# Kernel optimization log

Measured on AMD Instinct MI355X. Metric: run time of the kernel, lower is better.

Reference implementation:

```python
import jax, jax.numpy as jnp
import numpy as np

V, D, H, F, L, M, T, B, MAXT = 32000, 1024, 16, 4096, 3, 1, 1024, 2, 2048
HD = D // H

def _ln(x, g, b, eps=1e-5):
    m = x.mean(-1, keepdims=True)
    v = ((x - m) ** 2).mean(-1, keepdims=True)
    return (x - m) * jax.lax.rsqrt(v + eps) * g + b

def _mha(x, Wq, bq, Wk, bk, Wv, bv, Wo, bo, mask):
    Bx, Tx, Dx = x.shape
    q = (x @ Wq.T + bq).reshape(Bx, Tx, H, HD)
    k = (x @ Wk.T + bk).reshape(Bx, Tx, H, HD)
    v = (x @ Wv.T + bv).reshape(Bx, Tx, H, HD)
    s = jnp.einsum('bqhd,bkhd->bhqk', q, k) / np.float32(np.sqrt(HD))
    s = jnp.where(mask[None, None], s, jnp.float32(-1e9))
    a = jax.nn.softmax(s, axis=-1)
    o = jnp.einsum('bhqk,bkhd->bqhd', a, v).reshape(Bx, Tx, Dx)
    return o @ Wo.T + bo

def setup_inputs() -> dict:
    key = jax.random.key(0)
    ks = iter(jax.random.split(key, 64))
    rn = lambda shape: jax.random.normal(next(ks), shape, jnp.float32) * 0.02
    inp = {
        'x': jax.random.randint(next(ks), (B, T), 0, V),
        'mask': jnp.tril(jnp.ones((T, T), bool)),  # causal mask
        'tok_W': rn((V, D)),  # embedding table = Linear(V,D).weight.T
        'pos_embed': rn((MAXT, D)),
        'Wq': rn((L, D, D)), 'bq': jnp.zeros((L, D)),
        'Wk': rn((L, D, D)), 'bk': jnp.zeros((L, D)),
        'Wv': rn((L, D, D)), 'bv': jnp.zeros((L, D)),
        'Wo': rn((L, D, D)), 'bo': jnp.zeros((L, D)),
        'ln1_g': jnp.ones((L, D)), 'ln1_b': jnp.zeros((L, D)),
        'W1': rn((L, F, D)), 'b1': jnp.zeros((L, F)),
        'W2': rn((L, D, F)), 'b2': jnp.zeros((L, D)),
        'ln2_g': jnp.ones((L, D)), 'ln2_b': jnp.zeros((L, D)),
        'mWq': rn((M, D, D)), 'mbq': jnp.zeros((M, D)),
        'mWk': rn((M, D, D)), 'mbk': jnp.zeros((M, D)),
        'mWv': rn((M, D, D)), 'mbv': jnp.zeros((M, D)),
        'mWo': rn((M, D, D)), 'mbo': jnp.zeros((M, D)),
        'mln_g': jnp.ones((M, D)), 'mln_b': jnp.zeros((M, D)),
        'tWq': rn((D, D)), 'tbq': jnp.zeros((D,)),
        'tWk': rn((D, D)), 'tbk': jnp.zeros((D,)),
        'tWv': rn((D, D)), 'tbv': jnp.zeros((D,)),
        'tWo': rn((D, D)), 'tbo': jnp.zeros((D,)),
        'tln_g': jnp.ones((D,)), 'tln_b': jnp.zeros((D,)),
        'norm_g': jnp.ones((D,)), 'norm_b': jnp.zeros((D,)),
        'out_W': rn((V, D)), 'out_b': jnp.zeros((V,)),
    }
    return inp

def reference(x, mask, tok_W, pos_embed, Wq, bq, Wk, bk, Wv, bv, Wo, bo,
              ln1_g, ln1_b, W1, b1, W2, b2, ln2_g, ln2_b,
              mWq, mbq, mWk, mbk, mWv, mbv, mWo, mbo, mln_g, mln_b,
              tWq, tbq, tWk, tbk, tWv, tbv, tWo, tbo, tln_g, tln_b,
              norm_g, norm_b, out_W, out_b):
    Bx, Tx = x.shape
    # one_hot(x, V).float() @ W_tok^T  ==  gather row x from the (V, D) table
    h = jnp.take(tok_W, x, axis=0) + pos_embed[:Tx][None]
    mi = 0
    for i in range(L):  # static small layer count
        a = _mha(h, Wq[i], bq[i], Wk[i], bk[i], Wv[i], bv[i], Wo[i], bo[i], mask)
        h = _ln(h + a, ln1_g[i], ln1_b[i])
        f = jax.nn.gelu(h @ W1[i].T + b1[i]) @ W2[i].T + b2[i]
        h = _ln(h + f, ln2_g[i], ln2_b[i])
        if i % 3 == 2 and mi < M:  # memory layer every 3rd block
            a = _mha(h, mWq[mi], mbq[mi], mWk[mi], mbk[mi], mWv[mi], mbv[mi], mWo[mi], mbo[mi], mask)
            h = _ln(h + a, mln_g[mi], mln_b[mi])
            mi += 1
    a = _mha(h, tWq, tbq, tWk, tbk, tWv, tbv, tWo, tbo, mask)  # thought attention
    h = _ln(h + a, tln_g, tln_b)
    h = _ln(h, norm_g, norm_b)
    return h @ out_W.T + out_b  # [B, T, V] logits
```

## Files before the change

kernel.cpp:

```cpp
#include <hip/hip_runtime.h>
#include <cstdint>

#define DEV static __device__ __forceinline__

typedef unsigned short u16;
typedef __attribute__((ext_vector_type(8))) short short8;
typedef __attribute__((ext_vector_type(4))) float f32x4;

namespace cfg {
constexpr int V = 32000, D = 1024, H = 16, F = 4096, L = 3, T = 1024, B = 2;
constexpr int N = B * T;
constexpr int HD = D / H;
}

DEV float bf2f(u16 b) { union { unsigned u; float f; } x; x.u = (unsigned)b << 16; return x.f; }
DEV u16 f2bf(float f) {
  union { float f; unsigned u; } x; x.f = f;
  unsigned u = x.u;
  return (u16)((u + 0x7fffu + ((u >> 16) & 1u)) >> 16);
}

DEV void gload16(void* lds, const void* g) {
  __builtin_amdgcn_global_load_lds((__attribute__((address_space(1))) void*)g,
                                   (__attribute__((address_space(3))) void*)lds, 16, 0, 0);
}

DEV float waveSum(float v) {
#pragma unroll
  for (int o = 32; o; o >>= 1) v += __shfl_xor(v, o);
  return v;
}

struct CastJob { const float* src; u16* dst; int nBlk; };
struct CastArgs { CastJob j[24]; int n; };

__global__ void cast_kernel(CastArgs a) {
  int blk = blockIdx.x;
  int i = 0;
  while (i + 1 < a.n && blk >= a.j[i].nBlk) { blk -= a.j[i].nBlk; ++i; }
  const size_t base = (size_t)blk * 2048 + threadIdx.x * 8;
  const float4* s4 = (const float4*)(a.j[i].src + base);
  const float4 v0 = s4[0], v1 = s4[1];
  short8 o;
  o[0] = (short)f2bf(v0.x); o[1] = (short)f2bf(v0.y);
  o[2] = (short)f2bf(v0.z); o[3] = (short)f2bf(v0.w);
  o[4] = (short)f2bf(v1.x); o[5] = (short)f2bf(v1.y);
  o[6] = (short)f2bf(v1.z); o[7] = (short)f2bf(v1.w);
  *(short8*)(a.j[i].dst + base) = o;
}

struct CopyJob { const float* src; float* dst; };
struct CopyArgs { CopyJob j[16]; int n; };
__global__ void bconcat_kernel(CopyArgs a) {
  const CopyJob jb = a.j[blockIdx.x];
  ((float4*)jb.dst)[threadIdx.x] = ((const float4*)jb.src)[threadIdx.x];
}

__global__ void embed_kernel(const int* __restrict__ x, const float* __restrict__ tokW,
                             const float* __restrict__ pos, float* __restrict__ hF,
                             u16* __restrict__ hB) {
  const int bt = blockIdx.x;
  const int t = bt & (cfg::T - 1);
  const int tid = threadIdx.x;
  const int idx = x[bt];
  float4 v = ((const float4*)(tokW + (size_t)idx * cfg::D))[tid];
  const float4 p = ((const float4*)(pos + (size_t)t * cfg::D))[tid];
  v.x += p.x; v.y += p.y; v.z += p.z; v.w += p.w;
  ((float4*)(hF + (size_t)bt * cfg::D))[tid] = v;
  union { u16 u[4]; uint2 q; } pk;
  pk.u[0] = f2bf(v.x); pk.u[1] = f2bf(v.y); pk.u[2] = f2bf(v.z); pk.u[3] = f2bf(v.w);
  *(uint2*)(hB + (size_t)bt * cfg::D + tid * 4) = pk.q;
}

template <int NADD>
__global__ void ln_kernel(const float* __restrict__ base,
                          const float* __restrict__ a0, const float* __restrict__ a1,
                          const float* __restrict__ a2, const float* __restrict__ a3,
                          const float* __restrict__ biasv,
                          const float* __restrict__ g, const float* __restrict__ bt,
                          float* __restrict__ outF, u16* __restrict__ outB) {
  const int row = blockIdx.x, tid = threadIdx.x;
  const int lane = tid & 63, wid = tid >> 6;
  const size_t roff = (size_t)row * cfg::D;
  float4 x = ((const float4*)(base + roff))[tid];
  if (NADD >= 1) {
    const float4 a = ((const float4*)(a0 + roff))[tid];
    x.x += a.x; x.y += a.y; x.z += a.z; x.w += a.w;
  }
  if (NADD >= 2) {
    const float4 a = ((const float4*)(a1 + roff))[tid];
    x.x += a.x; x.y += a.y; x.z += a.z; x.w += a.w;
  }
  if (NADD >= 3) {
    const float4 a = ((const float4*)(a2 + roff))[tid];
    x.x += a.x; x.y += a.y; x.z += a.z; x.w += a.w;
  }
  if (NADD >= 4) {
    const float4 a = ((const float4*)(a3 + roff))[tid];
    x.x += a.x; x.y += a.y; x.z += a.z; x.w += a.w;
  }
  if (biasv) {
    const float4 a = ((const float4*)biasv)[tid];
    x.x += a.x; x.y += a.y; x.z += a.z; x.w += a.w;
  }
  float s = x.x + x.y + x.z + x.w;
  float s2 = x.x * x.x + x.y * x.y + x.z * x.z + x.w * x.w;
  __shared__ float sb[8];
  s = waveSum(s); s2 = waveSum(s2);
  if (lane == 0) { sb[wid] = s; sb[4 + wid] = s2; }
  __syncthreads();
  s = sb[0] + sb[1] + sb[2] + sb[3];
  s2 = sb[4] + sb[5] + sb[6] + sb[7];
  const float mean = s * (1.f / cfg::D);
  const float rs = rsqrtf(s2 * (1.f / cfg::D) - mean * mean + 1e-5f);
  const float4 gv = ((const float4*)g)[tid];
  const float4 bv = ((const float4*)bt)[tid];
  float4 y;
  y.x = (x.x - mean) * rs * gv.x + bv.x;
  y.y = (x.y - mean) * rs * gv.y + bv.y;
  y.z = (x.z - mean) * rs * gv.z + bv.z;
  y.w = (x.w - mean) * rs * gv.w + bv.w;
  ((float4*)(outF + roff))[tid] = y;
  union { u16 u[4]; uint2 q; } pk;
  pk.u[0] = f2bf(y.x); pk.u[1] = f2bf(y.y); pk.u[2] = f2bf(y.z); pk.u[3] = f2bf(y.w);
  *(uint2*)(outB + roff + tid * 4) = pk.q;
}

__global__ void vtrans_kernel(const u16* __restrict__ v, u16* __restrict__ vtO, int vstride) {
  __shared__ u16 s[64][68];
  const int bh = blockIdx.y, b = bh >> 4, h = bh & 15;
  const int t0 = blockIdx.x * 64;
  const int tid = threadIdx.x;
  const int r2 = tid >> 3, cg = tid & 7;
#pragma unroll
  for (int p = 0; p < 2; ++p) {
    const int r = p * 32 + r2;
    const short8 val = *(const short8*)(v + (size_t)(b * cfg::T + t0 + r) * vstride + h * 64 + cg * 8);
#pragma unroll
    for (int j = 0; j < 8; ++j) s[r][cg * 8 + j] = (u16)val[j];
  }
  __syncthreads();
#pragma unroll
  for (int p = 0; p < 2; ++p) {
    const int d = p * 32 + r2;
    short8 o;
#pragma unroll
    for (int j = 0; j < 8; ++j) o[j] = (short)s[cg * 8 + j][d];
    *(short8*)(vtO + ((size_t)bh * 64 + d) * (size_t)cfg::T + t0 + cg * 8) = o;
  }
}

template <int NCH>
DEV void stageTile(u16* lds, const u16* src, int strideElems, int tid) {
#pragma unroll
  for (int c = 0; c < NCH / 256; ++c) {
    const int ci = c * 256 + tid;
    const int r = ci >> 3;
    const int c8 = ci & 7;
    const int sc8 = c8 ^ (r & 7);
    gload16(lds + (size_t)ci * 8, src + (size_t)r * strideElems + sc8 * 8);
  }
}
DEV short8 ldsFrag(const u16* tile, int row, int kElem) {
  const int byteoff = row * 128 + ((kElem * 2) ^ ((row & 7) << 4));
  return *(const short8*)((const char*)tile + byteoff);
}

__launch_bounds__(256, 3)
__global__ void fattn_kernel(const u16* __restrict__ qkv, const u16* __restrict__ vt,
                             u16* __restrict__ o) {
  constexpr int D3 = 3 * cfg::D;
  __shared__ u16 Qs[64 * 64];
  __shared__ u16 Ks[64 * 64];
  __shared__ u16 Vs[64 * 64];
  __shared__ u16 Ps[64][72];
  const int tid = threadIdx.x, lane = tid & 63, w = tid >> 6;
  const int qt = gridDim.x - 1 - blockIdx.x;
  const int bh = blockIdx.y;
  const int b = bh >> 4, h = bh & 15;
  const int q0 = qt * 64;
  const int l15 = lane & 15, lq = lane >> 4;

  stageTile<512>(Qs, qkv + (size_t)(b * cfg::T + q0) * D3 + h * 64, D3, tid);
  __syncthreads();
  short8 qf[2];
#pragma unroll
  for (int kk = 0; kk < 2; ++kk)
    qf[kk] = ldsFrag(Qs, w * 16 + l15, kk * 32 + lq * 8);

  f32x4 oa[4];
  float m[4], l[4];
#pragma unroll
  for (int r = 0; r < 4; ++r) { m[r] = -1e30f; l[r] = 0.f; }
#pragma unroll
  for (int nt = 0; nt < 4; ++nt) { oa[nt][0] = 0; oa[nt][1] = 0; oa[nt][2] = 0; oa[nt][3] = 0; }

  const int nkt = qt + 1;
  const u16* kbase = qkv + (size_t)(b * cfg::T) * D3 + cfg::D + h * 64;
  const u16* vbase = vt + (size_t)bh * 64 * cfg::T;

  for (int kt = 0; kt < nkt; ++kt) {
    const int k0 = kt * 64;
    __syncthreads();
    stageTile<512>(Ks, kbase + (size_t)k0 * D3, D3, tid);
    stageTile<512>(Vs, vbase + k0, cfg::T, tid);
    __syncthreads();

    f32x4 sa[4];
#pragma unroll
    for (int nt = 0; nt < 4; ++nt) { sa[nt][0] = 0; sa[nt][1] = 0; sa[nt][2] = 0; sa[nt][3] = 0; }
#pragma unroll
    for (int kk = 0; kk < 2; ++kk) {
      short8 kf[4];
#pragma unroll
      for (int nt = 0; nt < 4; ++nt) kf[nt] = ldsFrag(Ks, nt * 16 + l15, kk * 32 + lq * 8);
#pragma unroll
      for (int nt = 0; nt < 4; ++nt)
        sa[nt] = __builtin_amdgcn_mfma_f32_16x16x32_bf16(qf[kk], kf[nt], sa[nt], 0, 0, 0);
    }

    const bool needMask = (kt >= qt);
#pragma unroll
    for (int r = 0; r < 4; ++r) {
      const int qrow = q0 + w * 16 + lq * 4 + r;
      float s[4];
#pragma unroll
      for (int nt = 0; nt < 4; ++nt) {
        s[nt] = sa[nt][r] * 0.125f;
        if (needMask && (k0 + nt * 16 + l15 > qrow)) s[nt] = -3e38f;
      }
      float rm = fmaxf(fmaxf(s[0], s[1]), fmaxf(s[2], s[3]));
#pragma unroll
      for (int off = 1; off < 16; off <<= 1) rm = fmaxf(rm, __shfl_xor(rm, off));
      const float mn = fmaxf(m[r], rm);
      const float sc = __expf(m[r] - mn);
      m[r] = mn;
      float ps = 0.f;
#pragma unroll
      for (int nt = 0; nt < 4; ++nt) {
        const float p = __expf(s[nt] - mn);
        ps += p;
        Ps[w * 16 + lq * 4 + r][nt * 16 + l15] = f2bf(p);
      }
#pragma unroll
      for (int off = 1; off < 16; off <<= 1) ps += __shfl_xor(ps, off);
      l[r] = l[r] * sc + ps;
#pragma unroll
      for (int nt = 0; nt < 4; ++nt) oa[nt][r] *= sc;
    }

#pragma unroll
    for (int kk = 0; kk < 2; ++kk) {
      short8 pa = *(const short8*)&Ps[w * 16 + l15][kk * 32 + lq * 8];
      short8 vf[4];
#pragma unroll
      for (int nt = 0; nt < 4; ++nt) vf[nt] = ldsFrag(Vs, nt * 16 + l15, kk * 32 + lq * 8);
#pragma unroll
      for (int nt = 0; nt < 4; ++nt)
        oa[nt] = __builtin_amdgcn_mfma_f32_16x16x32_bf16(pa, vf[nt], oa[nt], 0, 0, 0);
    }
  }

  u16* obase = o + (size_t)(b * cfg::T + q0 + w * 16) * cfg::D + h * 64;
#pragma unroll
  for (int r = 0; r < 4; ++r) {
    const float inv = 1.f / l[r];
    const int rl = lq * 4 + r;
#pragma unroll
    for (int nt = 0; nt < 4; ++nt)
      obase[(size_t)rl * cfg::D + nt * 16 + l15] = f2bf(oa[nt][r] * inv);
  }
}

template <int BN, int EPI, int OUTF32, int SWZ, int MMAJOR>
__launch_bounds__(256, 4)
__global__ void gemm_kernel(const u16* __restrict__ A, const u16* __restrict__ Bw,
                            const float* __restrict__ bias, void* __restrict__ Cp,
                            int lda, int ldb, int ldc, int K, long long partStride) {
  constexpr int BM = 128, BK = 64;
  constexpr int WN = BN / 2;
  constexpr int MF = 4, NF = WN / 16;
  int bx = blockIdx.x, by = blockIdx.y;
  if (SWZ) {
    const int gx = gridDim.x;
    const int nwg = gx * gridDim.y;
    const int lid = by * gx + bx;
    const int q = nwg >> 3, r = nwg & 7;
    const int xcd = lid & 7, rest = lid >> 3;
    const int nid = (xcd < r ? xcd * (q + 1) : r * (q + 1) + (xcd - r) * q) + rest;
    bx = nid % gx; by = nid / gx;
  }
  const int z = blockIdx.z;
  const u16* Ab = A + (size_t)z * K;
  const u16* Bb = Bw + (size_t)z * K;
  const int tid = threadIdx.x;
  const int lane = tid & 63;
  const int wid = tid >> 6;
  const int wr = wid >> 1, wc = wid & 1;
  const int m0 = (MMAJOR ? bx : by) * BM;
  const int n0 = (MMAJOR ? by : bx) * BN;

  __shared__ u16 As[BM][BK];
  __shared__ u16 Bs[BN][BK];

  const int nkt = K / BK;

  f32x4 acc[MF][NF];
#pragma unroll
  for (int i = 0; i < MF; ++i)
#pragma unroll
    for (int j = 0; j < NF; ++j) {
      acc[i][j][0] = 0.f; acc[i][j][1] = 0.f; acc[i][j][2] = 0.f; acc[i][j][3] = 0.f;
    }

  for (int kt = 0; kt < nkt; ++kt) {
    __syncthreads();
    const int kb = kt * BK;
    stageTile<(BM * BK) / 8>(&As[0][0], Ab + (size_t)m0 * lda + kb, lda, tid);
    stageTile<(BN * BK) / 8>(&Bs[0][0], Bb + (size_t)n0 * ldb + kb, ldb, tid);
    __syncthreads();
#pragma unroll
    for (int kk = 0; kk < BK / 32; ++kk) {
      short8 av[MF], bv[NF];
      const int kElem = kk * 32 + (lane >> 4) * 8;
#pragma unroll
      for (int mt = 0; mt < MF; ++mt)
        av[mt] = ldsFrag(&As[0][0], wr * 64 + mt * 16 + (lane & 15), kElem);
#pragma unroll
      for (int nt = 0; nt < NF; ++nt)
        bv[nt] = ldsFrag(&Bs[0][0], wc * WN + nt * 16 + (lane & 15), kElem);
#pragma unroll
      for (int mt = 0; mt < MF; ++mt)
#pragma unroll
        for (int nt = 0; nt < NF; ++nt)
          acc[mt][nt] = __builtin_amdgcn_mfma_f32_16x16x32_bf16(av[mt], bv[nt], acc[mt][nt], 0, 0, 0);
    }
  }

  const int rhi = (lane >> 4) * 4, cidx = lane & 15;
  const long long cb = (long long)z * partStride;
#pragma unroll
  for (int mt = 0; mt < MF; ++mt) {
#pragma unroll
    for (int nt = 0; nt < NF; ++nt) {
      const int col = n0 + wc * WN + nt * 16 + cidx;
      const float badd = bias ? bias[col] : 0.f;
#pragma unroll
      for (int r = 0; r < 4; ++r) {
        const int row = m0 + wr * 64 + mt * 16 + rhi + r;
        float val = acc[mt][nt][r] + badd;
        if (EPI == 1) {
          const float zz = 1.5957691216057308f * (val + 0.044715f * val * val * val);
          const float th = 1.f - 2.f / (__expf(zz) + 1.f);
          val = 0.5f * val * (1.f + th);
        }
        const size_t off = (size_t)(cb + (long long)row * ldc + col);
        if (OUTF32) ((float*)Cp)[off] = val;
        else ((u16*)Cp)[off] = f2bf(val);
      }
    }
  }
}

extern "C" void kernel_launch(void* const* d_in, const int* in_sizes, int n_in,
                              void* d_out, int out_size, void* d_ws, size_t ws_size,
                              hipStream_t stream) {
  using namespace cfg;
  (void)in_sizes; (void)n_in; (void)out_size;
  const int* x = (const int*)d_in[0];
  const float* tokW = (const float*)d_in[2];
  const float* pos = (const float*)d_in[3];
  const float* Wq = (const float*)d_in[4];  const float* bq = (const float*)d_in[5];
  const float* Wk = (const float*)d_in[6];  const float* bk = (const float*)d_in[7];
  const float* Wv = (const float*)d_in[8];  const float* bv = (const float*)d_in[9];
  const float* Wo = (const float*)d_in[10]; const float* bo = (const float*)d_in[11];
  const float* ln1g = (const float*)d_in[12]; const float* ln1b = (const float*)d_in[13];
  const float* W1 = (const float*)d_in[14]; const float* b1 = (const float*)d_in[15];
  const float* W2 = (const float*)d_in[16]; const float* b2 = (const float*)d_in[17];
  const float* ln2g = (const float*)d_in[18]; const float* ln2b = (const float*)d_in[19];
  const float* mWq = (const float*)d_in[20]; const float* mbq = (const float*)d_in[21];
  const float* mWk = (const float*)d_in[22]; const float* mbk = (const float*)d_in[23];
  const float* mWv = (const float*)d_in[24]; const float* mbv = (const float*)d_in[25];
  const float* mWo = (const float*)d_in[26]; const float* mbo = (const float*)d_in[27];
  const float* mlng = (const float*)d_in[28]; const float* mlnb = (const float*)d_in[29];
  const float* tWq = (const float*)d_in[30]; const float* tbq = (const float*)d_in[31];
  const float* tWk = (const float*)d_in[32]; const float* tbk = (const float*)d_in[33];
  const float* tWv = (const float*)d_in[34]; const float* tbv = (const float*)d_in[35];
  const float* tWo = (const float*)d_in[36]; const float* tbo = (const float*)d_in[37];
  const float* tlng = (const float*)d_in[38]; const float* tlnb = (const float*)d_in[39];
  const float* normg = (const float*)d_in[40]; const float* normb = (const float*)d_in[41];
  const float* outW = (const float*)d_in[42]; const float* outb = (const float*)d_in[43];

  const size_t DD = (size_t)D * D;
  const long long ND = (long long)N * D;
  char* wsb = (char*)d_ws;
  size_t off = 0;
  auto alloc = [&](size_t bytes) {
    void* p = wsb + off;
    off += (bytes + 255) & ~(size_t)255;
    return p;
  };
  u16* qkvW = (u16*)alloc((size_t)L * 3 * DD * 2);
  u16* mqkvW = (u16*)alloc(3 * DD * 2);
  u16* tqkvW = (u16*)alloc(3 * DD * 2);
  u16* WoB = (u16*)alloc((size_t)L * DD * 2);
  u16* W1B = (u16*)alloc((size_t)L * F * D * 2);
  u16* W2B = (u16*)alloc((size_t)L * D * F * 2);
  u16* mWoB = (u16*)alloc(DD * 2);
  u16* tWoB = (u16*)alloc(DD * 2);
  u16* outWB = (u16*)alloc((size_t)V * D * 2);
  float* biasQKV = (float*)alloc((size_t)(L + 2) * 3 * D * 4);
  float* hF = (float*)alloc((size_t)N * D * 4);
  u16* hB = (u16*)alloc((size_t)N * D * 2);
  float* pS = (float*)alloc((size_t)4 * N * D * 4);
  u16* qkvB = (u16*)alloc((size_t)N * 3 * D * 2);
  u16* vtB = (u16*)alloc((size_t)N * D * 2);
  u16* oB = (u16*)alloc((size_t)N * D * 2);
  u16* f1B = (u16*)alloc((size_t)N * F * 2);
  if (off > ws_size) return;

  CastArgs ca;
  int nj = 0; long total = 0;
  auto addJob = [&](const float* s, u16* dptr, size_t n) {
    ca.j[nj].src = s; ca.j[nj].dst = dptr; ca.j[nj].nBlk = (int)(n / 2048);
    total += (long)(n / 2048); ++nj;
  };
  for (int i = 0; i < L; ++i) {
    addJob(Wq + i * DD, qkvW + (size_t)i * 3 * DD, DD);
    addJob(Wk + i * DD, qkvW + (size_t)i * 3 * DD + DD, DD);
    addJob(Wv + i * DD, qkvW + (size_t)i * 3 * DD + 2 * DD, DD);
  }
  addJob(mWq, mqkvW, DD); addJob(mWk, mqkvW + DD, DD); addJob(mWv, mqkvW + 2 * DD, DD);
  addJob(tWq, tqkvW, DD); addJob(tWk, tqkvW + DD, DD); addJob(tWv, tqkvW + 2 * DD, DD);
  addJob(Wo, WoB, (size_t)L * DD);
  addJob(W1, W1B, (size_t)L * F * D);
  addJob(W2, W2B, (size_t)L * D * F);
  addJob(mWo, mWoB, DD); addJob(tWo, tWoB, DD);
  addJob(outW, outWB, (size_t)V * D);
  ca.n = nj;
  cast_kernel<<<dim3((unsigned)total), 256, 0, stream>>>(ca);

  CopyArgs cpa;
  int nc = 0;
  auto addCopy = [&](const float* s, float* dptr) { cpa.j[nc].src = s; cpa.j[nc].dst = dptr; ++nc; };
  for (int i = 0; i < L; ++i) {
    addCopy(bq + (size_t)i * D, biasQKV + (size_t)i * 3 * D);
    addCopy(bk + (size_t)i * D, biasQKV + (size_t)i * 3 * D + D);
    addCopy(bv + (size_t)i * D, biasQKV + (size_t)i * 3 * D + 2 * D);
  }
  addCopy(mbq, biasQKV + (size_t)L * 3 * D); addCopy(mbk, biasQKV + (size_t)L * 3 * D + D);
  addCopy(mbv, biasQKV + (size_t)L * 3 * D + 2 * D);
  addCopy(tbq, biasQKV + (size_t)(L + 1) * 3 * D); addCopy(tbk, biasQKV + (size_t)(L + 1) * 3 * D + D);
  addCopy(tbv, biasQKV + (size_t)(L + 1) * 3 * D + 2 * D);
  cpa.n = nc;
  bconcat_kernel<<<dim3((unsigned)nc), 256, 0, stream>>>(cpa);

  embed_kernel<<<N, 256, 0, stream>>>(x, tokW, pos, hF, hB);

  auto mha = [&](const u16* qkvw, const float* qkvbias, const u16* wo) {
    gemm_kernel<64, 0, 0, 0, 0><<<dim3(3 * D / 64, N / 128, 1), 256, 0, stream>>>(
        hB, qkvw, qkvbias, qkvB, D, D, 3 * D, D, 0);
    vtrans_kernel<<<dim3(T / 64, B * H), 256, 0, stream>>>(qkvB + 2 * D, vtB, 3 * D);
    fattn_kernel<<<dim3(T / 64, B * H), 256, 0, stream>>>(qkvB, vtB, oB);
    gemm_kernel<64, 0, 1, 0, 0><<<dim3(D / 64, N / 128, 4), 256, 0, stream>>>(
        oB, wo, nullptr, pS, D, D, D, 256, ND);
  };
  auto lnMha = [&](const float* obias, const float* g, const float* b_) {
    ln_kernel<4><<<N, 256, 0, stream>>>(hF, pS, pS + ND, pS + 2 * ND, pS + 3 * ND,
                                        obias, g, b_, hF, hB);
  };

  int mi = 0;
  for (int i = 0; i < L; ++i) {
    mha(qkvW + (size_t)i * 3 * DD, biasQKV + (size_t)i * 3 * D, WoB + (size_t)i * DD);
    lnMha(bo + (size_t)i * D, ln1g + (size_t)i * D, ln1b + (size_t)i * D);
    gemm_kernel<64, 1, 0, 0, 0><<<dim3(F / 64, N / 128, 1), 256, 0, stream>>>(
        hB, W1B + (size_t)i * F * D, b1 + (size_t)i * F, f1B, D, D, F, D, 0);
    gemm_kernel<64, 0, 1, 0, 0><<<dim3(D / 64, N / 128, 4), 256, 0, stream>>>(
        f1B, W2B + (size_t)i * D * F, nullptr, pS, F, F, D, 1024, ND);
    ln_kernel<4><<<N, 256, 0, stream>>>(hF, pS, pS + ND, pS + 2 * ND, pS + 3 * ND,
                                        b2 + (size_t)i * D, ln2g + (size_t)i * D,
                                        ln2b + (size_t)i * D, hF, hB);
    if (i % 3 == 2 && mi < 1) {
      mha(mqkvW, biasQKV + (size_t)L * 3 * D, mWoB);
      lnMha(mbo, mlng, mlnb);
      ++mi;
    }
  }
  mha(tqkvW, biasQKV + (size_t)(L + 1) * 3 * D, tWoB);
  lnMha(tbo, tlng, tlnb);
  ln_kernel<0><<<N, 256, 0, stream>>>(hF, nullptr, nullptr, nullptr, nullptr, nullptr,
                                      normg, normb, hF, hB);
  gemm_kernel<128, 0, 1, 1, 1><<<dim3(N / 128, V / 128, 1), 256, 0, stream>>>(
      hB, outWB, outb, (float*)d_out, D, D, V, D, 0);
}
```

Before: 929.2 us.

## Add 256x256-tile 4-stage pipelined GEMM for output logits projection

Adds a new GEMM kernel for the final vocabulary projection. It uses 256x256 tiles, 512 threads, a 4-buffer LDS ring that prefetches 3 stages ahead with explicit vmcnt waits and raw barriers, XCD-aware block remapping, and 16x16x32 bf16 MFMA. The aim is more data reuse per tile and overlap of global loads with MFMA on the largest GEMM. In exchange it needs 128KB of dynamic LDS, which allows only one block per CU. The older kernel is kept as a fallback if the shared-memory attribute cannot be set.

Result: faster. 906.0 us (-2.5%).

```diff
diff --git a/kernel.cpp b/kernel.cpp
--- a/kernel.cpp
+++ b/kernel.cpp
@@ -23,6 +23,23 @@
 DEV void gload16(void* lds, const void* g) {
   __builtin_amdgcn_global_load_lds((__attribute__((address_space(1))) void*)g,
                                    (__attribute__((address_space(3))) void*)lds, 16, 0, 0);
+}
+
+template <int NW>
+DEV void waitVm() {
+  if constexpr (NW == 0) asm volatile("s_waitcnt vmcnt(0)" ::: "memory");
+  else if constexpr (NW == 4) asm volatile("s_waitcnt vmcnt(4)" ::: "memory");
+  else if constexpr (NW == 8) asm volatile("s_waitcnt vmcnt(8)" ::: "memory");
+  __builtin_amdgcn_sched_barrier(0);
+}
+DEV void barrierRaw() {
+  __builtin_amdgcn_sched_barrier(0);
+  __builtin_amdgcn_s_barrier();
+  __builtin_amdgcn_sched_barrier(0);
+}
+DEV void waitLgkm0() {
+  asm volatile("s_waitcnt lgkmcnt(0)" ::: "memory");
+  __builtin_amdgcn_sched_barrier(0);
 }
 
 DEV float waveSum(float v) {
@@ -165,6 +182,10 @@
   const int byteoff = row * 128 + ((kElem * 2) ^ ((row & 7) << 4));
   return *(const short8*)((const char*)tile + byteoff);
 }
+DEV short8 ldsFrag32(const u16* tile, int row, int kElem) {
+  const int byteoff = row * 64 + ((kElem * 2) ^ (((row >> 1) & 3) << 4));
+  return *(const short8*)((const char*)tile + byteoff);
+}
 
 __launch_bounds__(256, 3)
 __global__ void fattn_kernel(const u16* __restrict__ qkv, const u16* __restrict__ vt,
@@ -357,6 +378,107 @@
         const size_t off = (size_t)(cb + (long long)row * ldc + col);
         if (OUTF32) ((float*)Cp)[off] = val;
         else ((u16*)Cp)[off] = f2bf(val);
+      }
+    }
+  }
+}
+
+__launch_bounds__(512, 1)
+__global__ void gemm256c_kernel(const u16* __restrict__ A, const u16* __restrict__ Bw,
+                                const float* __restrict__ bias, float* __restrict__ Cp,
+                                int lda, int ldb, int ldc, int K) {
+  extern __shared__ u16 lds[];
+  int bx = blockIdx.x, by = blockIdx.y;
+  {
+    const int gx = gridDim.x;
+    const int nwg = gx * gridDim.y;
+    const int lid = by * gx + bx;
+    const int q = nwg >> 3, r = nwg & 7;
+    const int xcd = lid & 7, rest = lid >> 3;
+    const int nid = (xcd < r ? xcd * (q + 1) : r * (q + 1) + (xcd - r) * q) + rest;
+    bx = nid % gx; by = nid / gx;
+  }
+  const int tid = threadIdx.x;
+  const int lane = tid & 63;
+  const int wid = tid >> 6;
+  const int wr = wid >> 2, wc = wid & 3;
+  const int m0 = bx * 256;
+  const int n0 = by * 256;
+  const int l15 = lane & 15, lq = lane >> 4;
+
+  const u16* Abase = A + (size_t)m0 * lda;
+  const u16* Bbase = Bw + (size_t)n0 * ldb;
+
+  auto stageHalf = [&](int ldsOff, const u16* srcBase, int ld, int kb, int h) {
+    const int ci = h * 512 + tid;
+    const int r = ci >> 2;
+    const int sc = (ci & 3) ^ ((r >> 1) & 3);
+    gload16(lds + ldsOff + (size_t)ci * 8, srcBase + (size_t)r * ld + kb + sc * 8);
+  };
+  auto stageA = [&](int buf, int kb) {
+    stageHalf(buf * 16384, Abase, lda, kb, 0);
+    stageHalf(buf * 16384, Abase, lda, kb, 1);
+  };
+  auto stageB = [&](int buf, int kb) {
+    stageHalf(buf * 16384 + 8192, Bbase, ldb, kb, 0);
+    stageHalf(buf * 16384 + 8192, Bbase, ldb, kb, 1);
+  };
+
+  f32x4 acc[8][4];
+#pragma unroll
+  for (int i = 0; i < 8; ++i)
+#pragma unroll
+    for (int j = 0; j < 4; ++j) { acc[i][j][0] = 0.f; acc[i][j][1] = 0.f; acc[i][j][2] = 0.f; acc[i][j][3] = 0.f; }
+
+  const int nt_ = K / 32;
+  for (int t = 0; t < 3; ++t) { stageA(t, t * 32); stageB(t, t * 32); }
+
+  const int kE = lq * 8;
+  for (int t = 0; t < nt_; ++t) {
+    if (t <= nt_ - 3) waitVm<8>();
+    else if (t == nt_ - 2) waitVm<4>();
+    else waitVm<0>();
+    barrierRaw();
+    const int buf = t & 3;
+    const u16* At = lds + buf * 16384;
+    const u16* Bt = lds + buf * 16384 + 8192;
+    const int nbuf = (t + 3) & 3;
+    const int kb3 = (t + 3) * 32;
+    const bool pf = (t + 3 < nt_);
+#pragma unroll
+    for (int mh = 0; mh < 2; ++mh) {
+      short8 av[4], bv[4];
+#pragma unroll
+      for (int mt = 0; mt < 4; ++mt)
+        av[mt] = ldsFrag32(At, wr * 128 + mh * 64 + mt * 16 + l15, kE);
+#pragma unroll
+      for (int nt = 0; nt < 4; ++nt)
+        bv[nt] = ldsFrag32(Bt, wc * 64 + nt * 16 + l15, kE);
+      if (pf) {
+        if (mh == 0) stageA(nbuf, kb3);
+        else stageB(nbuf, kb3);
+      }
+      waitLgkm0();
+      __builtin_amdgcn_s_setprio(1);
+#pragma unroll
+      for (int mt = 0; mt < 4; ++mt)
+#pragma unroll
+        for (int nt = 0; nt < 4; ++nt)
+          acc[mh * 4 + mt][nt] = __builtin_amdgcn_mfma_f32_16x16x32_bf16(av[mt], bv[nt], acc[mh * 4 + mt][nt], 0, 0, 0);
+      __builtin_amdgcn_s_setprio(0);
+    }
+  }
+
+#pragma unroll
+  for (int g = 0; g < 8; ++g) {
+#pragma unroll
+    for (int nt = 0; nt < 4; ++nt) {
+      const int col = n0 + wc * 64 + nt * 16 + l15;
+      const float badd = bias[col];
+#pragma unroll
+      for (int r = 0; r < 4; ++r) {
+        const int row = m0 + wr * 128 + g * 16 + lq * 4 + r;
+        Cp[(size_t)row * ldc + col] = acc[g][nt][r] + badd;
       }
     }
   }
@@ -491,6 +613,15 @@
   lnMha(tbo, tlng, tlnb);
   ln_kernel<0><<<N, 256, 0, stream>>>(hF, nullptr, nullptr, nullptr, nullptr, nullptr,
                                       normg, normb, hF, hB);
-  gemm_kernel<128, 0, 1, 1, 1><<<dim3(N / 128, V / 128, 1), 256, 0, stream>>>(
-      hB, outWB, outb, (float*)d_out, D, D, V, D, 0);
-}
+
+  hipError_t e = hipFuncSetAttribute(
+      reinterpret_cast<const void*>(gemm256c_kernel),
+      hipFuncAttributeMaxDynamicSharedMemorySize, 131072);
+  if (e == hipSuccess) {
+    gemm256c_kernel<<<dim3(N / 256, V / 256, 1), 512, 131072, stream>>>(
+        hB, outWB, outb, (float*)d_out, D, D, V, D);
+  } else {
+    gemm_kernel<128, 0, 1, 1, 1><<<dim3(N / 128, V / 128, 1), 256, 0, stream>>>(
+        hB, outWB, outb, (float*)d_out, D, D, V, D, 0);
+  }
+}
```
